# Kernel optimization log

Hardware: AMD Instinct MI355X
Metric: run time of the kernel (lower is better)

Reference implementation:

```python
import jax, jax.numpy as jnp
import numpy as np

N, E, D, H = 50000, 500000, 128, 4
HD = D // H
LN_EPS = 1e-5


def _layernorm(z, g, b):
    mu = jnp.mean(z, axis=-1, keepdims=True)
    var = jnp.mean(jnp.square(z - mu), axis=-1, keepdims=True)
    return (z - mu) * jax.lax.rsqrt(var + LN_EPS) * g + b


def setup_inputs() -> dict:
    key = jax.random.key(0)
    ks = jax.random.split(key, 10)
    s = 1.0 / np.sqrt(D)
    return {
        "x": jax.random.normal(ks[0], (N, D), jnp.float32),
        "edge_index": jax.random.randint(ks[1], (2, E), 0, N, jnp.int32),
        "edge_attr": jax.random.normal(ks[2], (E, D), jnp.float32),
        "W_l": jax.random.normal(ks[3], (D, D), jnp.float32) * s,
        "b_l": jnp.zeros((D,), jnp.float32),
        "W_r": jax.random.normal(ks[4], (D, D), jnp.float32) * s,
        "b_r": jnp.zeros((D,), jnp.float32),
        "W_e": jax.random.normal(ks[5], (D, D), jnp.float32) * s,
        "b_e": jnp.zeros((D,), jnp.float32),
        "att": jax.random.normal(ks[6], (H, HD), jnp.float32) * s,
        "bias": jnp.zeros((D,), jnp.float32),
        "ln_g": jnp.ones((2 * D,), jnp.float32),
        "ln_b": jnp.zeros((2 * D,), jnp.float32),
        "W_mlp": jax.random.normal(ks[7], (2 * D, D), jnp.float32) * (1.0 / np.sqrt(2 * D)),
        "b_mlp": jnp.zeros((D,), jnp.float32),
    }


def reference(x, edge_index, edge_attr, W_l, b_l, W_r, b_r, W_e, b_e, att,
              bias, ln_g, ln_b, W_mlp, b_mlp):
    n = x.shape[0]
    src, dst = edge_index[0], edge_index[1]
    # GATv2Conv (heads=H, concat=True, edge_dim=D)
    xl = (x @ W_l + b_l).reshape(n, H, HD)          # lin_l(x)
    xr = (x @ W_r + b_r).reshape(n, H, HD)          # lin_r(x)
    ee = (edge_attr @ W_e + b_e).reshape(-1, H, HD)  # lin_edge(edge_attr)
    m = xl[src] + xr[dst] + ee                       # [E,H,HD]
    e = jnp.sum(jax.nn.leaky_relu(m, 0.2) * att, axis=-1)  # [E,H]
    emax = jax.ops.segment_max(e, dst, num_segments=n)
    emax = jax.lax.stop_gradient(jnp.where(jnp.isfinite(emax), emax, 0.0))
    ex = jnp.exp(e - emax[dst])
    denom = jax.ops.segment_sum(ex, dst, num_segments=n)
    alpha = ex / (denom[dst] + 1e-16)                # segment softmax over incoming edges
    agg = jax.ops.segment_sum(alpha[..., None] * xl[src], dst, num_segments=n)
    x_new = agg.reshape(n, H * HD) + bias            # [N,D]
    # edgeMLP: gather -> concat -> LayerNorm -> ReLU -> Linear -> residual add
    cat = jnp.concatenate([x_new[src], x_new[dst]], axis=-1)  # [E,2D]
    h = jax.nn.relu(_layernorm(cat, ln_g, ln_b))
    edge_attr_new = edge_attr + h @ W_mlp + b_mlp
    return x_new, edge_attr_new
```

## Files before the change

kernel.cpp:

```cpp
#include <hip/hip_runtime.h>
#include <math.h>

typedef float  f32x4  __attribute__((ext_vector_type(4)));
typedef __bf16 bf16x8 __attribute__((ext_vector_type(8)));

union FragU { uint4 q; bf16x8 b; };

__device__ inline float fc(const float4& v, int k){
  return k==0 ? v.x : k==1 ? v.y : k==2 ? v.z : v.w;
}

__global__ void k_pack(const float* __restrict__ Wl, const float* __restrict__ Wr,
                       const float* __restrict__ We, const float* __restrict__ Wm,
                       const float* __restrict__ lng, const float* __restrict__ lnb,
                       unsigned short* plr, unsigned short* pe, unsigned short* pm,
                       unsigned short* plnb){
  int t = blockIdx.x * 256 + threadIdx.x;
  if (t < 32768){
    int j = t & 7, lane = (t >> 3) & 63, ks = (t >> 9) & 3, ct = t >> 11;
    int k = ks*32 + (lane >> 4)*8 + j, c = ct*16 + (lane & 15);
    float v = (c < 128) ? Wl[k*128 + c] : Wr[k*128 + (c - 128)];
    __bf16 b = (__bf16)v; plr[t] = *(unsigned short*)&b;
  }
  if (t < 16384){
    int j = t & 7, lane = (t >> 3) & 63, ks = (t >> 9) & 3, ct = t >> 11;
    int k = ks*32 + (lane >> 4)*8 + j, c = ct*16 + (lane & 15);
    __bf16 b = (__bf16)We[k*128 + c]; pe[t] = *(unsigned short*)&b;
  }
  if (t < 32768){
    int j = t & 7, lane = (t >> 3) & 63, ks = (t >> 9) & 7, ct = t >> 12;
    int k = ks*32 + (lane >> 4)*8 + j, c = ct*16 + (lane & 15);
    __bf16 b = (__bf16)Wm[k*128 + c]; pm[t] = *(unsigned short*)&b;
  }
  if (t < 512){
    float v = (t < 256) ? lng[t] : lnb[t-256];
    __bf16 b = (__bf16)v; plnb[t] = *(unsigned short*)&b;
  }
}

__global__ void k_scan1(const int* __restrict__ cnt, int* __restrict__ pre,
                        int* __restrict__ bsum, int n){
  __shared__ int wsum[4];
  int t = threadIdx.x, lane = t & 63, w = t >> 6;
  int base = blockIdx.x*1024 + t*4;
  int v[4]; int loc = 0;
  #pragma unroll
  for (int j = 0; j < 4; ++j){ v[j] = (base+j < n) ? cnt[base+j] : 0; loc += v[j]; }
  int incl = loc;
  #pragma unroll
  for (int o = 1; o < 64; o <<= 1){
    int u = __shfl_up(incl, o);
    if (lane >= o) incl += u;
  }
  if (lane == 63) wsum[w] = incl;
  __syncthreads();
  int wbase = 0;
  #pragma unroll
  for (int ww = 0; ww < 4; ++ww) if (ww < w) wbase += wsum[ww];
  int run = wbase + incl - loc;
  #pragma unroll
  for (int j = 0; j < 4; ++j){ if (base+j < n) pre[base+j] = run; run += v[j]; }
  if (t == 255) bsum[blockIdx.x] = wbase + incl;
}

__global__ void k_scan2(const int* __restrict__ bsum, int* __restrict__ boff, int nb){
  int t = threadIdx.x;
  int v = (t < nb) ? bsum[t] : 0;
  int incl = v;
  #pragma unroll
  for (int o = 1; o < 64; o <<= 1){
    int u = __shfl_up(incl, o);
    if (t >= o) incl += u;
  }
  if (t < nb) boff[t] = incl - v;
  if (t == nb-1) boff[nb] = incl;
}

__global__ void k_scan3(const int* __restrict__ pre, const int* __restrict__ boff,
                        int* __restrict__ rowptr, int* __restrict__ cursor, int n, int nb){
  int i = blockIdx.x*256 + threadIdx.x;
  if (i < n){
    int r = pre[i] + boff[blockIdx.x >> 2];
    rowptr[i] = r; cursor[i] = r;
  }
  if (i == 0) rowptr[n] = boff[nb];
}

__global__ void k_scatter(const int* __restrict__ dst, int* __restrict__ cursor,
                          int* __restrict__ eids, int E){
  int e = blockIdx.x*256 + threadIdx.x;
  if (e < E){ int p = atomicAdd(&cursor[dst[e]], 1); eids[p] = e; }
}

__launch_bounds__(512)
__global__ void k_node_linear(const float* __restrict__ x, const float* __restrict__ bl,
                              const float* __restrict__ br, const unsigned short* __restrict__ plr,
                              __bf16* __restrict__ xlxr, int n){
  __shared__ uint4 sW[4096];
  int t = threadIdx.x, lane = t & 63, w = t >> 6, lo = lane & 15, hi = lane >> 4;
  for (int i = t; i < 4096; i += 512) sW[i] = ((const uint4*)plr)[i];
  int row = blockIdx.x*128 + w*16 + lo;
  int rc  = min(row, n-1);
  bf16x8 A[4];
  #pragma unroll
  for (int ks = 0; ks < 4; ++ks){
    const float* p = &x[(size_t)rc*128 + ks*32 + hi*8];
    float4 v0 = *(const float4*)p, v1 = *(const float4*)(p+4);
    FragU u;
    u.b[0]=(__bf16)v0.x; u.b[1]=(__bf16)v0.y; u.b[2]=(__bf16)v0.z; u.b[3]=(__bf16)v0.w;
    u.b[4]=(__bf16)v1.x; u.b[5]=(__bf16)v1.y; u.b[6]=(__bf16)v1.z; u.b[7]=(__bf16)v1.w;
    A[ks] = u.b;
  }
  __syncthreads();
  f32x4 acc[16];
  #pragma unroll
  for (int ct = 0; ct < 16; ++ct) acc[ct] = (f32x4)(0.f);
  #pragma unroll
  for (int ks = 0; ks < 4; ++ks){
    #pragma unroll
    for (int ct = 0; ct < 16; ++ct){
      FragU bu; bu.q = sW[(ct*4 + ks)*64 + lane];
      acc[ct] = __builtin_amdgcn_mfma_f32_16x16x32_bf16(A[ks], bu.b, acc[ct], 0, 0, 0);
    }
  }
  float biasL[16];
  #pragma unroll
  for (int ct = 0; ct < 16; ++ct){
    int c = ct*16 + lo;
    biasL[ct] = (c < 128) ? bl[c] : br[c - 128];
  }
  #pragma unroll
  for (int j = 0; j < 4; ++j){
    int nd = blockIdx.x*128 + w*16 + hi*4 + j;
    if (nd < n){
      #pragma unroll
      for (int ct = 0; ct < 16; ++ct)
        xlxr[(size_t)nd*256 + ct*16 + lo] = (__bf16)(acc[ct][j] + biasL[ct]);
    }
  }
}

__launch_bounds__(512)
__global__ void k_edge_logits(const float* __restrict__ eattr, const int* __restrict__ src,
                              const int* __restrict__ dst, const unsigned short* __restrict__ pe,
                              const float* __restrict__ be, const float* __restrict__ att,
                              const __bf16* __restrict__ xlxr, float* __restrict__ elog,
                              int* __restrict__ cnt, int E){
  __shared__ uint4 sW[2048];
  int t = threadIdx.x, lane = t & 63, w = t >> 6, lo = lane & 15, hi = lane >> 4;
  for (int i = t; i < 2048; i += 512) sW[i] = ((const uint4*)pe)[i];
  int eb = blockIdx.x*128 + w*16;
  int er = min(eb + lo, E-1);
  bf16x8 A[4];
  #pragma unroll
  for (int ks = 0; ks < 4; ++ks){
    const float* p = &eattr[(size_t)er*128 + ks*32 + hi*8];
    f32x4 v0 = __builtin_nontemporal_load((const f32x4*)p);
    f32x4 v1 = __builtin_nontemporal_load((const f32x4*)(p+4));
    FragU u;
    u.b[0]=(__bf16)v0[0]; u.b[1]=(__bf16)v0[1]; u.b[2]=(__bf16)v0[2]; u.b[3]=(__bf16)v0[3];
    u.b[4]=(__bf16)v1[0]; u.b[5]=(__bf16)v1[1]; u.b[6]=(__bf16)v1[2]; u.b[7]=(__bf16)v1[3];
    A[ks] = u.b;
  }
  __syncthreads();
  f32x4 acc[8];
  #pragma unroll
  for (int ct = 0; ct < 8; ++ct) acc[ct] = (f32x4)(0.f);
  #pragma unroll
  for (int ks = 0; ks < 4; ++ks){
    #pragma unroll
    for (int ct = 0; ct < 8; ++ct){
      FragU bu; bu.q = sW[(ct*4 + ks)*64 + lane];
      acc[ct] = __builtin_amdgcn_mfma_f32_16x16x32_bf16(A[ks], bu.b, acc[ct], 0, 0, 0);
    }
  }
  float beL[8], atL[8];
  #pragma unroll
  for (int ct = 0; ct < 8; ++ct){ beL[ct] = be[ct*16 + lo]; atL[ct] = att[ct*16 + lo]; }
  #pragma unroll
  for (int j = 0; j < 4; ++j){
    int e = eb + hi*4 + j;
    int ec = min(e, E-1);
    int s_ = src[ec], d_ = dst[ec];
    const __bf16* xlp = &xlxr[(size_t)s_*256];
    const __bf16* xrp = &xlxr[(size_t)d_*256 + 128];
    float qh[4];
    #pragma unroll
    for (int h = 0; h < 4; ++h){
      float p = 0.f;
      #pragma unroll
      for (int u = 0; u < 2; ++u){
        int ct = 2*h + u, c = ct*16 + lo;
        float m = acc[ct][j] + beL[ct] + (float)xlp[c] + (float)xrp[c];
        m = (m > 0.f) ? m : 0.2f*m;
        p = fmaf(m, atL[ct], p);
      }
      p += __shfl_xor(p, 1); p += __shfl_xor(p, 2);
      p += __shfl_xor(p, 4); p += __shfl_xor(p, 8);
      qh[h] = p;
    }
    if (lo == 0 && e < E){
      *(float4*)&elog[(size_t)e*4] = make_float4(qh[0], qh[1], qh[2], qh[3]);
      atomicAdd(&cnt[d_], 1);
    }
  }
}

__launch_bounds__(256)
__global__ void k_gat_agg(const float* __restrict__ elog, const int* __restrict__ rowptr,
                          const int* __restrict__ eids, const int* __restrict__ src,
                          const __bf16* __restrict__ xlxr, const float* __restrict__ bias,
                          float* __restrict__ xnew, __bf16* __restrict__ xnb,
                          float2* __restrict__ nstat, int n){
  int nd = (blockIdx.x*256 + threadIdx.x) >> 6;
  int lane = threadIdx.x & 63;
  if (nd >= n) return;
  int beg = rowptr[nd], end = rowptr[nd+1];
  bool hsel = (lane & 32) != 0;
  float m0 = -INFINITY, m1 = -INFINITY;
  for (int i = beg; i < end; ++i){
    float4 lv = *(const float4*)&elog[(size_t)eids[i]*4];
    float l0 = hsel ? lv.y : lv.x, l1 = hsel ? lv.w : lv.z;
    m0 = fmaxf(m0, l0); m1 = fmaxf(m1, l1);
  }
  float d0 = 0.f, d1 = 0.f, a0 = 0.f, a1 = 0.f;
  int c0 = lane, c1 = lane + 64;
  for (int i = beg; i < end; ++i){
    int e = eids[i];
    float4 lv = *(const float4*)&elog[(size_t)e*4];
    float l0 = hsel ? lv.y : lv.x, l1 = hsel ? lv.w : lv.z;
    float e0 = __expf(l0 - m0), e1 = __expf(l1 - m1);
    d0 += e0; d1 += e1;
    const __bf16* xp = &xlxr[(size_t)src[e]*256];
    a0 = fmaf(e0, (float)xp[c0], a0);
    a1 = fmaf(e1, (float)xp[c1], a1);
  }
  float r0 = 1.f/(d0 + 1e-16f), r1 = 1.f/(d1 + 1e-16f);
  float v0 = fmaf(a0, r0, bias[c0]), v1 = fmaf(a1, r1, bias[c1]);
  xnew[(size_t)nd*128 + c0] = v0;
  xnew[(size_t)nd*128 + c1] = v1;
  xnb[(size_t)nd*128 + c0] = (__bf16)v0;
  xnb[(size_t)nd*128 + c1] = (__bf16)v1;
  float s  = v0 + v1;
  float ss = fmaf(v0, v0, v1*v1);
  #pragma unroll
  for (int o = 1; o < 64; o <<= 1){ s += __shfl_xor(s, o); ss += __shfl_xor(ss, o); }
  if (lane == 0) nstat[nd] = make_float2(s, ss);
}

__launch_bounds__(512, 4)
__global__ void k_edge_mlp(const __bf16* __restrict__ xnb, const int* __restrict__ src,
                           const int* __restrict__ dst, const float* __restrict__ eattr,
                           const unsigned short* __restrict__ pm, const float* __restrict__ bmlp,
                           const unsigned short* __restrict__ plnb,
                           const float2* __restrict__ nstat, float* __restrict__ out, int E){
  __shared__ uint4 sW[4096];
  __shared__ __align__(16) unsigned short sLN[512];
  const uint4* pm_q = (const uint4*)pm;
  int t = threadIdx.x, lane = t & 63, w = t >> 6, lo = lane & 15, hi = lane >> 4;
  int base = blockIdx.x*128;
  float ev[4][8];
  #pragma unroll
  for (int j = 0; j < 4; ++j){
    int e2 = min(base + w*16 + hi*4 + j, E-1);
    const float* ep = &eattr[(size_t)e2*128 + lo];
    #pragma unroll
    for (int ct = 0; ct < 8; ++ct)
      ev[j][ct] = __builtin_nontemporal_load(ep + ct*16);
  }
  for (int i = t; i < 4096; i += 512) sW[i] = pm_q[i];
  if (t < 512) sLN[t] = plnb[t];
  int e  = base + w*16 + lo;
  int ec = min(e, E-1);
  int s_ = src[ec], d_ = dst[ec];
  float2 stS = nstat[s_], stD = nstat[d_];
  float mean = (stS.x + stD.x) * (1.f/256.f);
  float var  = (stS.y + stD.y) * (1.f/256.f) - mean*mean;
  float rstd = rsqrtf(var + 1e-5f);
  const __bf16* srow = &xnb[(size_t)s_*128 + hi*8];
  const __bf16* drow = &xnb[(size_t)d_*128 + hi*8];
  uint4 g[8];
  #pragma unroll
  for (int ks = 0; ks < 4; ++ks){
    g[ks]   = *(const uint4*)&srow[ks*32];
    g[4+ks] = *(const uint4*)&drow[ks*32];
  }
  __syncthreads();
  bf16x8 af[8];
  #pragma unroll
  for (int ks = 0; ks < 8; ++ks){
    int cb = ks*32 + hi*8;
    FragU u, a, lg, lb;
    u.q  = g[ks];
    lg.q = *(const uint4*)&sLN[cb];
    lb.q = *(const uint4*)&sLN[256 + cb];
    #pragma unroll
    for (int j = 0; j < 8; ++j){
      float v = fmaxf(fmaf(((float)u.b[j] - mean)*rstd, (float)lg.b[j], (float)lb.b[j]), 0.f);
      a.b[j] = (__bf16)v;
    }
    af[ks] = a.b;
  }
  f32x4 acc[8];
  #pragma unroll
  for (int ct = 0; ct < 8; ++ct) acc[ct] = (f32x4)(0.f);
  #pragma unroll
  for (int ks = 0; ks < 8; ++ks){
    #pragma unroll
    for (int ct = 0; ct < 8; ++ct){
      FragU bu; bu.q = sW[(ct*8 + ks)*64 + lane];
      acc[ct] = __builtin_amdgcn_mfma_f32_16x16x32_bf16(af[ks], bu.b, acc[ct], 0, 0, 0);
    }
  }
  float bmL[8];
  #pragma unroll
  for (int ct = 0; ct < 8; ++ct) bmL[ct] = bmlp[ct*16 + lo];
  #pragma unroll
  for (int j = 0; j < 4; ++j){
    int e2 = base + w*16 + hi*4 + j;
    if (e2 < E){
      #pragma unroll
      for (int ct = 0; ct < 8; ++ct){
        int c = ct*16 + lo;
        __builtin_nontemporal_store(acc[ct][j] + bmL[ct] + ev[j][ct],
                                    &out[(size_t)e2*128 + c]);
      }
    }
  }
}

extern "C" void kernel_launch(void* const* d_in, const int* in_sizes, int n_in,
                              void* d_out, int out_size, void* d_ws, size_t ws_size,
                              hipStream_t stream){
  const float* x     = (const float*)d_in[0];
  const int*   eidx  = (const int*)  d_in[1];
  const float* eattr = (const float*)d_in[2];
  const float* Wl    = (const float*)d_in[3];
  const float* bl    = (const float*)d_in[4];
  const float* Wr    = (const float*)d_in[5];
  const float* br    = (const float*)d_in[6];
  const float* We    = (const float*)d_in[7];
  const float* be    = (const float*)d_in[8];
  const float* att   = (const float*)d_in[9];
  const float* bias  = (const float*)d_in[10];
  const float* lng   = (const float*)d_in[11];
  const float* lnb   = (const float*)d_in[12];
  const float* Wmlp  = (const float*)d_in[13];
  const float* bmlp  = (const float*)d_in[14];

  int n = in_sizes[0] / 128;
  int E = in_sizes[2] / 128;
  const int* src = eidx;
  const int* dst = eidx + E;
  int nb = (n + 1023) / 1024;

  char* ws = (char*)d_ws;
  size_t off = 0;
  int* cnt    = (int*)(ws + off); off += (size_t)n*4;
  size_t zbytes = off;
  int* pre    = (int*)(ws + off); off += (size_t)n*4;
  int* rowptr = (int*)(ws + off); off += (size_t)(n+1)*4;
  int* cursor = (int*)(ws + off); off += (size_t)(n+1)*4;
  int* bsum   = (int*)(ws + off); off += (size_t)nb*4;
  int* boff   = (int*)(ws + off); off += (size_t)(nb+1)*4;
  int* eids   = (int*)(ws + off); off += (size_t)E*4;
  __bf16* xlxr = (__bf16*)(ws + off); off += (size_t)n*256*2;
  float* elog = (float*)(ws + off); off += (size_t)E*4*4;
  float2* nstat = (float2*)(ws + off); off += (size_t)n*8;
  __bf16* xnb = (__bf16*)(ws + off); off += (size_t)n*128*2;
  unsigned short* plr = (unsigned short*)(ws + off); off += 32768*2;
  unsigned short* pe  = (unsigned short*)(ws + off); off += 16384*2;
  unsigned short* pm  = (unsigned short*)(ws + off); off += 32768*2;
  unsigned short* plnb= (unsigned short*)(ws + off); off += 512*2;

  float* xnew_out = (float*)d_out;
  float* eout     = (float*)d_out + (size_t)n*128;

  hipMemsetAsync(ws, 0, zbytes, stream);
  k_pack       <<<128, 256, 0, stream>>>(Wl, Wr, We, Wmlp, lng, lnb, plr, pe, pm, plnb);
  k_node_linear<<<(n + 127)/128, 512, 0, stream>>>(x, bl, br, plr, xlxr, n);
  k_edge_logits<<<(E + 127)/128, 512, 0, stream>>>(eattr, src, dst, pe, be, att, xlxr, elog, cnt, E);
  k_scan1      <<<nb, 256, 0, stream>>>(cnt, pre, bsum, n);
  k_scan2      <<<1, 64, 0, stream>>>(bsum, boff, nb);
  k_scan3      <<<nb*4, 256, 0, stream>>>(pre, boff, rowptr, cursor, n, nb);
  k_scatter    <<<(E + 255)/256, 256, 0, stream>>>(dst, cursor, eids, E);
  k_gat_agg    <<<(n + 3)/4, 256, 0, stream>>>(elog, rowptr, eids, src, xlxr, bias, xnew_out, xnb, nstat, n);
  k_edge_mlp   <<<(E + 127)/128, 512, 0, stream>>>(xnb, src, dst, eattr, pm, bmlp, plnb, nstat, eout, E);
}
```

Baseline: 442.5 us.

## Scatter edge logits and sources into CSR order, unroll aggregation by two

The scatter kernel now writes each edge's four logits and source index directly into dst-sorted arrays instead of writing only edge ids. The aggregation kernel then reads them contiguously, removing the indirect eids lookup and the random gathers of elog and src in both softmax passes. The max and accumulate loops are also unrolled by two so more independent loads are in flight. The cost is extra scattered writes (20 bytes per edge) in the scatter kernel and more workspace.

Measured after the change: 374.7 us, median of 3. -15.3%, faster.

```diff
diff --git a/kernel.cpp b/kernel.cpp
--- a/kernel.cpp
+++ b/kernel.cpp
@@ -86,10 +86,15 @@
   if (i == 0) rowptr[n] = boff[nb];
 }
 
-__global__ void k_scatter(const int* __restrict__ dst, int* __restrict__ cursor,
-                          int* __restrict__ eids, int E){
+__global__ void k_scatter(const int* __restrict__ dst, const int* __restrict__ src,
+                          const float* __restrict__ elog, int* __restrict__ cursor,
+                          float4* __restrict__ elogp, int* __restrict__ srcp, int E){
   int e = blockIdx.x*256 + threadIdx.x;
-  if (e < E){ int p = atomicAdd(&cursor[dst[e]], 1); eids[p] = e; }
+  if (e < E){
+    int p = atomicAdd(&cursor[dst[e]], 1);
+    elogp[p] = *(const float4*)&elog[(size_t)e*4];
+    srcp[p]  = src[e];
+  }
 }
 
 __launch_bounds__(512)
@@ -207,8 +212,8 @@
 }
 
 __launch_bounds__(256)
-__global__ void k_gat_agg(const float* __restrict__ elog, const int* __restrict__ rowptr,
-                          const int* __restrict__ eids, const int* __restrict__ src,
+__global__ void k_gat_agg(const float4* __restrict__ elogp, const int* __restrict__ rowptr,
+                          const int* __restrict__ srcp,
                           const __bf16* __restrict__ xlxr, const float* __restrict__ bias,
                           float* __restrict__ xnew, __bf16* __restrict__ xnb,
                           float2* __restrict__ nstat, int n){
@@ -218,20 +223,42 @@
   int beg = rowptr[nd], end = rowptr[nd+1];
   bool hsel = (lane & 32) != 0;
   float m0 = -INFINITY, m1 = -INFINITY;
-  for (int i = beg; i < end; ++i){
-    float4 lv = *(const float4*)&elog[(size_t)eids[i]*4];
-    float l0 = hsel ? lv.y : lv.x, l1 = hsel ? lv.w : lv.z;
-    m0 = fmaxf(m0, l0); m1 = fmaxf(m1, l1);
-  }
+  float m0b = -INFINITY, m1b = -INFINITY;
+  int i = beg;
+  for (; i + 1 < end; i += 2){
+    float4 la = elogp[i], lb = elogp[i+1];
+    float a0 = hsel ? la.y : la.x, a1 = hsel ? la.w : la.z;
+    float b0 = hsel ? lb.y : lb.x, b1 = hsel ? lb.w : lb.z;
+    m0 = fmaxf(m0, a0); m1 = fmaxf(m1, a1);
+    m0b = fmaxf(m0b, b0); m1b = fmaxf(m1b, b1);
+  }
+  if (i < end){
+    float4 la = elogp[i];
+    m0 = fmaxf(m0, hsel ? la.y : la.x); m1 = fmaxf(m1, hsel ? la.w : la.z);
+  }
+  m0 = fmaxf(m0, m0b); m1 = fmaxf(m1, m1b);
   float d0 = 0.f, d1 = 0.f, a0 = 0.f, a1 = 0.f;
   int c0 = lane, c1 = lane + 64;
-  for (int i = beg; i < end; ++i){
-    int e = eids[i];
-    float4 lv = *(const float4*)&elog[(size_t)e*4];
-    float l0 = hsel ? lv.y : lv.x, l1 = hsel ? lv.w : lv.z;
-    float e0 = __expf(l0 - m0), e1 = __expf(l1 - m1);
+  i = beg;
+  for (; i + 1 < end; i += 2){
+    float4 la = elogp[i], lb = elogp[i+1];
+    int spA = srcp[i], spB = srcp[i+1];
+    const __bf16* xpA = &xlxr[(size_t)spA*256];
+    const __bf16* xpB = &xlxr[(size_t)spB*256];
+    float xA0 = (float)xpA[c0], xA1 = (float)xpA[c1];
+    float xB0 = (float)xpB[c0], xB1 = (float)xpB[c1];
+    float eA0 = __expf((hsel ? la.y : la.x) - m0), eA1 = __expf((hsel ? la.w : la.z) - m1);
+    float eB0 = __expf((hsel ? lb.y : lb.x) - m0), eB1 = __expf((hsel ? lb.w : lb.z) - m1);
+    d0 += eA0 + eB0; d1 += eA1 + eB1;
+    a0 = fmaf(eA0, xA0, a0); a0 = fmaf(eB0, xB0, a0);
+    a1 = fmaf(eA1, xA1, a1); a1 = fmaf(eB1, xB1, a1);
+  }
+  if (i < end){
+    float4 la = elogp[i];
+    int sp = srcp[i];
+    const __bf16* xp = &xlxr[(size_t)sp*256];
+    float e0 = __expf((hsel ? la.y : la.x) - m0), e1 = __expf((hsel ? la.w : la.z) - m1);
     d0 += e0; d1 += e1;
-    const __bf16* xp = &xlxr[(size_t)src[e]*256];
     a0 = fmaf(e0, (float)xp[c0], a0);
     a1 = fmaf(e1, (float)xp[c1], a1);
   }
@@ -363,7 +390,9 @@
   int* cursor = (int*)(ws + off); off += (size_t)(n+1)*4;
   int* bsum   = (int*)(ws + off); off += (size_t)nb*4;
   int* boff   = (int*)(ws + off); off += (size_t)(nb+1)*4;
-  int* eids   = (int*)(ws + off); off += (size_t)E*4;
+  off = (off + 15) & ~(size_t)15;
+  float4* elogp = (float4*)(ws + off); off += (size_t)E*16;
+  int* srcp   = (int*)(ws + off); off += (size_t)E*4;
   __bf16* xlxr = (__bf16*)(ws + off); off += (size_t)n*256*2;
   float* elog = (float*)(ws + off); off += (size_t)E*4*4;
   float2* nstat = (float2*)(ws + off); off += (size_t)n*8;
@@ -383,7 +412,7 @@
   k_scan1      <<<nb, 256, 0, stream>>>(cnt, pre, bsum, n);
   k_scan2      <<<1, 64, 0, stream>>>(bsum, boff, nb);
   k_scan3      <<<nb*4, 256, 0, stream>>>(pre, boff, rowptr, cursor, n, nb);
-  k_scatter    <<<(E + 255)/256, 256, 0, stream>>>(dst, cursor, eids, E);
-  k_gat_agg    <<<(n + 3)/4, 256, 0, stream>>>(elog, rowptr, eids, src, xlxr, bias, xnew_out, xnb, nstat, n);
+  k_scatter    <<<(E + 255)/256, 256, 0, stream>>>(dst, src, elog, cursor, elogp, srcp, E);
+  k_gat_agg    <<<(n + 3)/4, 256, 0, stream>>>(elogp, rowptr, srcp, xlxr, bias, xnew_out, xnb, nstat, n);
   k_edge_mlp   <<<(E + 127)/128, 512, 0, stream>>>(xnb, src, dst, eattr, pm, bmlp, plnb, nstat, eout, E);
 }
```
